# Kernel optimization log

Measured on AMD Instinct MI355X. Metric: run time of the kernel, lower is better.

The kernel has to match this reference:

```python
import jax, jax.numpy as jnp
import numpy as np

D_MODEL = 1024
NUM_HEADS = 16
D_HEAD = D_MODEL // NUM_HEADS


def setup_inputs() -> dict:
    key = jax.random.key(0)
    k1, k2, k3, k4, k5 = jax.random.split(key, 5)
    s = 1.0 / np.sqrt(D_MODEL)
    return {
        "x": jax.random.normal(k1, (4, 2048, D_MODEL), dtype=jnp.float32),
        "W_qkv": jax.random.normal(k2, (D_MODEL, 3 * D_MODEL), dtype=jnp.float32) * s,
        "b_qkv": jnp.zeros((3 * D_MODEL,), dtype=jnp.float32),
        "W_out": jax.random.normal(k3, (D_MODEL, D_MODEL), dtype=jnp.float32) * s,
        "b_out": jnp.zeros((D_MODEL,), dtype=jnp.float32),
    }


def reference(x, W_qkv, b_qkv, W_out, b_out):
    B, T, D = x.shape
    qkv = x @ W_qkv + b_qkv  # [B,T,3D]
    q, k, v = jnp.split(qkv, 3, axis=-1)
    # [B,T,D] -> [B,H,T,dh]
    def to_heads(t):
        return t.reshape(B, T, NUM_HEADS, D_HEAD).transpose(0, 2, 1, 3)
    q, k, v = to_heads(q), to_heads(k), to_heads(v)
    scores = jnp.einsum("bhqd,bhkd->bhqk", q, k) / jnp.sqrt(jnp.float32(D_HEAD))
    attn = jax.nn.softmax(scores, axis=-1)
    out = jnp.einsum("bhqk,bhkd->bhqd", attn, v)
    out = out.transpose(0, 2, 1, 3).reshape(B, T, D)
    return out @ W_out + b_out
```

## Files before the change

### kernel.cpp

```cpp
#include <hip/hip_runtime.h>

typedef unsigned short u16;
typedef unsigned int u32;
typedef u16 u16x4 __attribute__((ext_vector_type(4)));
typedef u16 u16x8 __attribute__((ext_vector_type(8)));
typedef u32 u32x2 __attribute__((ext_vector_type(2)));
typedef u32 u32x4 __attribute__((ext_vector_type(4)));
typedef __bf16 bf16x2 __attribute__((ext_vector_type(2)));
typedef __bf16 bf16x8 __attribute__((ext_vector_type(8)));
typedef float f32x4 __attribute__((ext_vector_type(4)));

__device__ __forceinline__ u16 f2bf(float f) {
  return __builtin_bit_cast(u16, (__bf16)f);
}

__device__ __forceinline__ u32 packbf2(float lo, float hi) {
  bf16x2 t;
  t[0] = (__bf16)lo;
  t[1] = (__bf16)hi;
  return __builtin_bit_cast(u32, t);
}

__device__ __forceinline__ f32x4 mfma16(bf16x8 a, bf16x8 b, f32x4 c) {
  return __builtin_amdgcn_mfma_f32_16x16x32_bf16(a, b, c, 0, 0, 0);
}

#define GLOAD_LDS16(gsrc, ldst)                                              \
  __builtin_amdgcn_global_load_lds(                                          \
      (const __attribute__((address_space(1))) void*)(gsrc),                 \
      (__attribute__((address_space(3))) void*)(ldst), 16, 0, 0)

__global__ __launch_bounds__(256) void cvt_x(const float* __restrict__ in,
                                             u16* __restrict__ out, int n) {
  int i = (blockIdx.x * 256 + threadIdx.x) * 8;
  if (i >= n) return;
  u16x8 o;
#pragma unroll
  for (int j = 0; j < 8; j++) o[j] = f2bf(in[i + j]);
  *(u16x8*)&out[i] = o;
}

__global__ __launch_bounds__(256) void transpose_cvt(const float* __restrict__ in,
                                                     u16* __restrict__ out,
                                                     int R, int C) {
  __shared__ float tile[32][33];
  int gx = blockIdx.x * 32, gy = blockIdx.y * 32;
  int tx = threadIdx.x, ty = threadIdx.y;
#pragma unroll
  for (int i = 0; i < 4; i++)
    tile[ty + i * 8][tx] = in[(size_t)(gy + ty + i * 8) * C + gx + tx];
  __syncthreads();
#pragma unroll
  for (int i = 0; i < 4; i++) {
    int c = ty + i * 8;
    out[(size_t)(gx + c) * R + gy + tx] = f2bf(tile[tx][c]);
  }
}

template <int EPI, int GX>
__global__ __launch_bounds__(256, 4) void gemm_bf16(
    const u16* __restrict__ A, const u16* __restrict__ Bt,
    const float* __restrict__ bias, u16* __restrict__ qb, u16* __restrict__ kb,
    u16* __restrict__ vb, float* __restrict__ fout, int N, int K) {
  __shared__ u16 As[2][128 * 32];
  __shared__ u16 Bs[2][128 * 32];
  const int tid = threadIdx.x;
  const int wave = tid >> 6;
  const int lane = tid & 63;
  const int wr = wave >> 1, wc = wave & 1;
  const int l15 = lane & 15, l4 = lane >> 4;

  const int id = blockIdx.y * GX + blockIdx.x;
  const int xcd = id & 7;
  const int j = id >> 3;
  const int bm = (xcd * 8 + j / GX) * 128;
  const int bn = (j % GX) * 128;

  const int srow = wave * 16 + (lane >> 2);
  const int slch = lane & 3;
  const int ldst = wave * 512;

  const u16* Abase = A + (size_t)bm * K;
  const u16* Bbase = Bt + (size_t)bn * K;

  f32x4 acc[4][4] = {};

  auto STAGE = [&](int buf, int k0) {
#pragma unroll
    for (int c = 0; c < 2; c++) {
      const int row = c * 64 + srow;
      const int sch = slch ^ ((row >> 1) & 3);
      GLOAD_LDS16(Abase + (size_t)row * K + k0 + sch * 8,
                  &As[buf][c * 2048 + ldst]);
      GLOAD_LDS16(Bbase + (size_t)row * K + k0 + sch * 8,
                  &Bs[buf][c * 2048 + ldst]);
    }
  };

  STAGE(0, 0);
  int cur = 0;
  for (int k0 = 0; k0 < K; k0 += 32) {
    __syncthreads();
    if (k0 + 32 < K) STAGE(cur ^ 1, k0 + 32);

    const u16* as = As[cur];
    const u16* bs = Bs[cur];
    bf16x8 af[4], bfr[4];
#pragma unroll
    for (int mi = 0; mi < 4; mi++) {
      const int row = wr * 64 + mi * 16 + l15;
      af[mi] = *(const bf16x8*)&as[row * 32 + ((l4 ^ ((row >> 1) & 3)) * 8)];
    }
#pragma unroll
    for (int ni = 0; ni < 4; ni++) {
      const int row = wc * 64 + ni * 16 + l15;
      bfr[ni] = *(const bf16x8*)&bs[row * 32 + ((l4 ^ ((row >> 1) & 3)) * 8)];
    }
    __builtin_amdgcn_s_setprio(1);
#pragma unroll
    for (int mi = 0; mi < 4; mi++)
#pragma unroll
      for (int ni = 0; ni < 4; ni++)
        acc[mi][ni] = mfma16(af[mi], bfr[ni], acc[mi][ni]);
    __builtin_amdgcn_s_setprio(0);
    cur ^= 1;
  }

#pragma unroll
  for (int mi = 0; mi < 4; mi++) {
#pragma unroll
    for (int ni = 0; ni < 4; ni++) {
      const int col = bn + wc * 64 + ni * 16 + l15;
      const float bv = bias[col];
      const int row0 = bm + wr * 64 + mi * 16 + l4 * 4;
      if (EPI == 0) {
        const int which = col >> 10;
        const int hc = col & 1023;
        const int h = hc >> 6, d = hc & 63;
#pragma unroll
        for (int r = 0; r < 4; r++) {
          const int row = row0 + r;
          const int b = row >> 11, t = row & 2047;
          const float v = acc[mi][ni][r] + bv;
          if (which == 0)
            qb[((size_t)(b * 16 + h) * 2048 + t) * 64 + d] = f2bf(v * 0.18033688f);
          else if (which == 1)
            kb[((size_t)(b * 16 + h) * 2048 + t) * 64 + d] = f2bf(v);
          else {
            const int o = t & 63;
            const int op = (o & 3) | (((o >> 4) & 1) << 2) | (((o >> 2) & 3) << 3) |
                           ((o >> 5) << 5);
            const int tp = (t & ~63) | op;
            vb[((size_t)(b * 16 + h) * 64 + d) * 2048 + tp] = f2bf(v);
          }
        }
      } else {
#pragma unroll
        for (int r = 0; r < 4; r++)
          fout[(size_t)(row0 + r) * N + col] = acc[mi][ni][r] + bv;
      }
    }
  }
}

__global__ __launch_bounds__(256, 4) void attn_kernel(const u16* __restrict__ Q,
                                                      const u16* __restrict__ Kg,
                                                      const u16* __restrict__ Vt,
                                                      u16* __restrict__ O) {
  __shared__ u16 Ks[2][64 * 64];
  __shared__ u16 Vs[2][64 * 64];
  const int tid = threadIdx.x;
  const int wave = tid >> 6;
  const int lane = tid & 63;
  const int l15 = lane & 15, l4 = lane >> 4;

  const int id = blockIdx.y * 16 + blockIdx.x;
  const int xcd = id & 7;
  const int j = id >> 3;
  const int bh = xcd * 8 + (j >> 4);
  const int qt = j & 15;

  const u16* qg = Q + ((size_t)bh * 2048 + qt * 128 + wave * 32) * 64;
  bf16x8 qf[2][2];
#pragma unroll
  for (int mi = 0; mi < 2; mi++)
#pragma unroll
    for (int kg2 = 0; kg2 < 2; kg2++)
      qf[mi][kg2] = *(const bf16x8*)&qg[(mi * 16 + l15) * 64 + kg2 * 32 + l4 * 8];

  float mrow[2] = {-1e30f, -1e30f};
  float lrow[2] = {0.f, 0.f};
  f32x4 oacc[4][2] = {};

  const int srow = wave * 8 + (lane >> 3);
  const int slch = lane & 7;
  const int ldst = wave * 512;
  const u16* kbase = Kg + (size_t)bh * 2048 * 64;
  const u16* vbase = Vt + (size_t)bh * 64 * 2048;

  auto STAGE = [&](int buf, int kt) {
#pragma unroll
    for (int c = 0; c < 2; c++) {
      const int row = c * 32 + srow;
      const int sch = slch ^ (row & 7);
      GLOAD_LDS16(kbase + (size_t)(kt * 64 + row) * 64 + sch * 8,
                  &Ks[buf][c * 2048 + ldst]);
      GLOAD_LDS16(vbase + (size_t)row * 2048 + kt * 64 + sch * 8,
                  &Vs[buf][c * 2048 + ldst]);
    }
  };

  STAGE(0, 0);
  int cur = 0;
  for (int kt = 0; kt < 32; kt++) {
    __syncthreads();
    if (kt + 1 < 32) STAGE(cur ^ 1, kt + 1);
    const u16* ks = Ks[cur];
    const u16* vs = Vs[cur];

    f32x4 sacc[2][4] = {};
    __builtin_amdgcn_s_setprio(1);
#pragma unroll
    for (int kg2 = 0; kg2 < 2; kg2++) {
#pragma unroll
      for (int ni = 0; ni < 4; ni++) {
        const int row = ni * 16 + l15;
        bf16x8 kf =
            *(const bf16x8*)&ks[row * 64 + (((kg2 * 4 + l4) ^ (row & 7)) * 8)];
#pragma unroll
        for (int mi = 0; mi < 2; mi++)
          sacc[mi][ni] = mfma16(kf, qf[mi][kg2], sacc[mi][ni]);
      }
    }
    __builtin_amdgcn_s_setprio(0);

#pragma unroll
    for (int mi = 0; mi < 2; mi++) {
      float pm0 = fmaxf(fmaxf(sacc[mi][0][0], sacc[mi][0][1]),
                        fmaxf(sacc[mi][0][2], sacc[mi][0][3]));
      float pm1 = fmaxf(fmaxf(sacc[mi][1][0], sacc[mi][1][1]),
                        fmaxf(sacc[mi][1][2], sacc[mi][1][3]));
      float pm2 = fmaxf(fmaxf(sacc[mi][2][0], sacc[mi][2][1]),
                        fmaxf(sacc[mi][2][2], sacc[mi][2][3]));
      float pm3 = fmaxf(fmaxf(sacc[mi][3][0], sacc[mi][3][1]),
                        fmaxf(sacc[mi][3][2], sacc[mi][3][3]));
      float pm = fmaxf(fmaxf(pm0, pm1), fmaxf(pm2, pm3));
      pm = fmaxf(pm, __shfl_xor(pm, 16));
      pm = fmaxf(pm, __shfl_xor(pm, 32));
      const bool noskip = !__all(pm - mrow[mi] <= 6.0f);
      float mnew = mrow[mi];
      if (noskip) {
        mnew = fmaxf(mrow[mi], pm);
        const float alpha = __builtin_amdgcn_exp2f(mrow[mi] - mnew);
        mrow[mi] = mnew;
        lrow[mi] *= alpha;
#pragma unroll
        for (int di = 0; di < 4; di++) oacc[di][mi] *= alpha;
      }
      float rs = 0.f;
#pragma unroll
      for (int ni = 0; ni < 4; ni++)
#pragma unroll
        for (int r = 0; r < 4; r++) {
          const float p = __builtin_amdgcn_exp2f(sacc[mi][ni][r] - mnew);
          sacc[mi][ni][r] = p;
          rs += p;
        }
      rs += __shfl_xor(rs, 16);
      rs += __shfl_xor(rs, 32);
      lrow[mi] += rs;
    }

#pragma unroll
    for (int kg2 = 0; kg2 < 2; kg2++) {
      bf16x8 pf[2];
#pragma unroll
      for (int mi = 0; mi < 2; mi++) {
        u32x4 praw;
        praw[0] = packbf2(sacc[mi][2 * kg2][0], sacc[mi][2 * kg2][1]);
        praw[1] = packbf2(sacc[mi][2 * kg2][2], sacc[mi][2 * kg2][3]);
        praw[2] = packbf2(sacc[mi][2 * kg2 + 1][0], sacc[mi][2 * kg2 + 1][1]);
        praw[3] = packbf2(sacc[mi][2 * kg2 + 1][2], sacc[mi][2 * kg2 + 1][3]);
        pf[mi] = __builtin_bit_cast(bf16x8, praw);
      }
      __builtin_amdgcn_s_setprio(1);
#pragma unroll
      for (int di = 0; di < 4; di++) {
        const int row = di * 16 + l15;
        bf16x8 vf =
            *(const bf16x8*)&vs[row * 64 + (((kg2 * 4 + l4) ^ (row & 7)) * 8)];
#pragma unroll
        for (int mi = 0; mi < 2; mi++)
          oacc[di][mi] = mfma16(vf, pf[mi], oacc[di][mi]);
      }
      __builtin_amdgcn_s_setprio(0);
    }
    cur ^= 1;
  }

  const int b = bh >> 4, h = bh & 15;
#pragma unroll
  for (int mi = 0; mi < 2; mi++) {
    const float invl = 1.0f / lrow[mi];
    const int t = qt * 128 + wave * 32 + mi * 16 + l15;
#pragma unroll
    for (int di = 0; di < 4; di++) {
      u16x4 o;
#pragma unroll
      for (int r = 0; r < 4; r++) o[r] = f2bf(oacc[di][mi][r] * invl);
      *(u16x4*)&O[((size_t)b * 2048 + t) * 1024 + h * 64 + di * 16 + l4 * 4] = o;
    }
  }
}

extern "C" void kernel_launch(void* const* d_in, const int* in_sizes, int n_in,
                              void* d_out, int out_size, void* d_ws, size_t ws_size,
                              hipStream_t stream) {
  const float* x = (const float*)d_in[0];
  const float* Wqkv = (const float*)d_in[1];
  const float* bqkv = (const float*)d_in[2];
  const float* Wout = (const float*)d_in[3];
  const float* bout = (const float*)d_in[4];
  float* out = (float*)d_out;

  u16* ws = (u16*)d_ws;
  u16* xb = ws;
  u16* wqT = xb + 8388608;
  u16* woT = wqT + 3145728;
  u16* qb = woT + 1048576;
  u16* kb = qb + 8388608;
  u16* vb = kb + 8388608;
  u16* ao = vb + 8388608;

  cvt_x<<<4096, 256, 0, stream>>>(x, xb, 8388608);
  transpose_cvt<<<dim3(96, 32), dim3(32, 8), 0, stream>>>(Wqkv, wqT, 1024, 3072);
  transpose_cvt<<<dim3(32, 32), dim3(32, 8), 0, stream>>>(Wout, woT, 1024, 1024);
  gemm_bf16<0, 24><<<dim3(24, 64), 256, 0, stream>>>(xb, wqT, bqkv, qb, kb, vb,
                                                     nullptr, 3072, 1024);
  attn_kernel<<<dim3(16, 64), 256, 0, stream>>>(qb, kb, vb, ao);
  gemm_bf16<1, 8><<<dim3(8, 64), 256, 0, stream>>>(ao, woT, bout, nullptr,
                                                   nullptr, nullptr, out, 1024, 1024);
}
```

Measured before the change: 223.4 us.

## Replace 128x128 GEMM with 256x256 tile, 8-wave ping-pong pipelined kernel

Replaces the 128x128 bf16 GEMM with a 256x256-tile kernel using 512 threads, 128KB dynamic LDS split into four double-buffered pieces, and explicit barrier and vmcnt scheduling. Global loads are interleaved with MFMA phases. The goal is more operand reuse per byte loaded and better overlap of loads with compute. The cost is one block per CU and fewer blocks overall: 384 for QKV and only 128 for the output projection, which underfills 256 CUs.

```diff
diff --git a/kernel.cpp b/kernel.cpp
--- a/kernel.cpp
+++ b/kernel.cpp
@@ -30,6 +30,13 @@
       (const __attribute__((address_space(1))) void*)(gsrc),                 \
       (__attribute__((address_space(3))) void*)(ldst), 16, 0, 0)
 
+#define SBAR()                                                               \
+  do {                                                                       \
+    __builtin_amdgcn_sched_barrier(0);                                       \
+    __builtin_amdgcn_s_barrier();                                            \
+    __builtin_amdgcn_sched_barrier(0);                                       \
+  } while (0)
+
 __global__ __launch_bounds__(256) void cvt_x(const float* __restrict__ in,
                                              u16* __restrict__ out, int n) {
   int i = (blockIdx.x * 256 + threadIdx.x) * 8;
@@ -57,82 +64,135 @@
   }
 }
 
-template <int EPI, int GX>
-__global__ __launch_bounds__(256, 4) void gemm_bf16(
+template <int EPI>
+__global__ __launch_bounds__(512, 1) void gemm256(
     const u16* __restrict__ A, const u16* __restrict__ Bt,
     const float* __restrict__ bias, u16* __restrict__ qb, u16* __restrict__ kb,
-    u16* __restrict__ vb, float* __restrict__ fout, int N, int K) {
-  __shared__ u16 As[2][128 * 32];
-  __shared__ u16 Bs[2][128 * 32];
+    u16* __restrict__ vb, float* __restrict__ fout, int N, int K, int NBN) {
+  extern __shared__ u16 lds[];
   const int tid = threadIdx.x;
-  const int wave = tid >> 6;
+  const int wid = tid >> 6;
   const int lane = tid & 63;
-  const int wr = wave >> 1, wc = wave & 1;
+  const int wr = wid >> 2, wc = wid & 3;
   const int l15 = lane & 15, l4 = lane >> 4;
 
-  const int id = blockIdx.y * GX + blockIdx.x;
-  const int xcd = id & 7;
-  const int j = id >> 3;
-  const int bm = (xcd * 8 + j / GX) * 128;
-  const int bn = (j % GX) * 128;
-
-  const int srow = wave * 16 + (lane >> 2);
-  const int slch = lane & 3;
-  const int ldst = wave * 512;
-
-  const u16* Abase = A + (size_t)bm * K;
-  const u16* Bbase = Bt + (size_t)bn * K;
-
-  f32x4 acc[4][4] = {};
-
-  auto STAGE = [&](int buf, int k0) {
+  const int nb = gridDim.x;
+  const int id2 = (blockIdx.x & 7) * (nb >> 3) + (blockIdx.x >> 3);
+  const int bm = (id2 / NBN) * 256;
+  const int bn = (id2 % NBN) * 256;
+
+  const u16* Ab = A + (size_t)bm * K;
+  const u16* Bb = Bt + (size_t)bn * K;
+
+#define PIECE(p, b) (lds + (p) * 16384 + (b) * 8192)
+
+  const int srow = wid * 16 + (lane >> 2);
+  const int sch0 = lane & 3;
+
+  auto STAGE1 = [&](u16* dst, const u16* srcb, int kofs) {
 #pragma unroll
     for (int c = 0; c < 2; c++) {
-      const int row = c * 64 + srow;
-      const int sch = slch ^ ((row >> 1) & 3);
-      GLOAD_LDS16(Abase + (size_t)row * K + k0 + sch * 8,
-                  &As[buf][c * 2048 + ldst]);
-      GLOAD_LDS16(Bbase + (size_t)row * K + k0 + sch * 8,
-                  &Bs[buf][c * 2048 + ldst]);
+      const int row = c * 128 + srow;
+      const int sch = sch0 ^ (row & 3) ^ ((row >> 2) & 3);
+      GLOAD_LDS16(srcb + (size_t)row * K + kofs + sch * 8, dst + c * 4096 + tid * 8);
     }
   };
-
-  STAGE(0, 0);
-  int cur = 0;
-  for (int k0 = 0; k0 < K; k0 += 32) {
-    __syncthreads();
-    if (k0 + 32 < K) STAGE(cur ^ 1, k0 + 32);
-
-    const u16* as = As[cur];
-    const u16* bs = Bs[cur];
-    bf16x8 af[4], bfr[4];
-#pragma unroll
-    for (int mi = 0; mi < 4; mi++) {
-      const int row = wr * 64 + mi * 16 + l15;
-      af[mi] = *(const bf16x8*)&as[row * 32 + ((l4 ^ ((row >> 1) & 3)) * 8)];
-    }
-#pragma unroll
-    for (int ni = 0; ni < 4; ni++) {
-      const int row = wc * 64 + ni * 16 + l15;
-      bfr[ni] = *(const bf16x8*)&bs[row * 32 + ((l4 ^ ((row >> 1) & 3)) * 8)];
-    }
+  auto RDA = [&](const u16* arr, int mi) -> bf16x8 {
+    const int row = wr * 128 + mi * 16 + l15;
+    const int ch = l4 ^ (row & 3) ^ ((row >> 2) & 3);
+    return *(const bf16x8*)&arr[row * 32 + ch * 8];
+  };
+  auto RDB = [&](const u16* arr, int ni) -> bf16x8 {
+    const int row = wc * 64 + ni * 16 + l15;
+    const int ch = l4 ^ (row & 3) ^ ((row >> 2) & 3);
+    return *(const bf16x8*)&arr[row * 32 + ch * 8];
+  };
+
+  f32x4 acc[8][4] = {};
+
+  STAGE1(PIECE(0, 0), Ab, 0);
+  STAGE1(PIECE(2, 0), Bb, 0);
+  STAGE1(PIECE(1, 0), Ab, 32);
+  STAGE1(PIECE(3, 0), Bb, 32);
+  asm volatile("s_waitcnt vmcnt(4)" ::: "memory");
+  SBAR();
+
+  const int NT = K >> 6;
+  for (int t = 0; t < NT; ++t) {
+    const int buf = t & 1, nbuf = buf ^ 1;
+    const int knext = (t + 1) << 6;
+    const bool pre = (t + 1 < NT);
+    bf16x8 af[8], bfr[2];
+
+#pragma unroll
+    for (int mi = 0; mi < 8; mi++) af[mi] = RDA(PIECE(0, buf), mi);
+    bfr[0] = RDB(PIECE(2, buf), 0);
+    bfr[1] = RDB(PIECE(2, buf), 1);
+    if (pre) STAGE1(PIECE(0, nbuf), Ab, knext);
+    SBAR();
     __builtin_amdgcn_s_setprio(1);
 #pragma unroll
-    for (int mi = 0; mi < 4; mi++)
-#pragma unroll
-      for (int ni = 0; ni < 4; ni++)
-        acc[mi][ni] = mfma16(af[mi], bfr[ni], acc[mi][ni]);
+    for (int mi = 0; mi < 8; mi++) {
+      acc[mi][0] = mfma16(af[mi], bfr[0], acc[mi][0]);
+      acc[mi][1] = mfma16(af[mi], bfr[1], acc[mi][1]);
+    }
     __builtin_amdgcn_s_setprio(0);
-    cur ^= 1;
+    SBAR();
+
+    bfr[0] = RDB(PIECE(2, buf), 2);
+    bfr[1] = RDB(PIECE(2, buf), 3);
+    if (pre) STAGE1(PIECE(2, nbuf), Bb, knext);
+    SBAR();
+    __builtin_amdgcn_s_setprio(1);
+#pragma unroll
+    for (int mi = 0; mi < 8; mi++) {
+      acc[mi][2] = mfma16(af[mi], bfr[0], acc[mi][2]);
+      acc[mi][3] = mfma16(af[mi], bfr[1], acc[mi][3]);
+    }
+    __builtin_amdgcn_s_setprio(0);
+    if (pre)
+      asm volatile("s_waitcnt vmcnt(4)" ::: "memory");
+    else
+      asm volatile("s_waitcnt vmcnt(0)" ::: "memory");
+    SBAR();
+
+#pragma unroll
+    for (int mi = 0; mi < 8; mi++) af[mi] = RDA(PIECE(1, buf), mi);
+    bfr[0] = RDB(PIECE(3, buf), 0);
+    bfr[1] = RDB(PIECE(3, buf), 1);
+    if (pre) STAGE1(PIECE(1, nbuf), Ab, knext + 32);
+    SBAR();
+    __builtin_amdgcn_s_setprio(1);
+#pragma unroll
+    for (int mi = 0; mi < 8; mi++) {
+      acc[mi][0] = mfma16(af[mi], bfr[0], acc[mi][0]);
+      acc[mi][1] = mfma16(af[mi], bfr[1], acc[mi][1]);
+    }
+    __builtin_amdgcn_s_setprio(0);
+    SBAR();
+
+    bfr[0] = RDB(PIECE(3, buf), 2);
+    bfr[1] = RDB(PIECE(3, buf), 3);
+    if (pre) STAGE1(PIECE(3, nbuf), Bb, knext + 32);
+    SBAR();
+    __builtin_amdgcn_s_setprio(1);
+#pragma unroll
+    for (int mi = 0; mi < 8; mi++) {
+      acc[mi][2] = mfma16(af[mi], bfr[0], acc[mi][2]);
+      acc[mi][3] = mfma16(af[mi], bfr[1], acc[mi][3]);
+    }
+    __builtin_amdgcn_s_setprio(0);
+    if (pre) asm volatile("s_waitcnt vmcnt(4)" ::: "memory");
+    SBAR();
   }
 
 #pragma unroll
-  for (int mi = 0; mi < 4; mi++) {
+  for (int mi = 0; mi < 8; mi++) {
 #pragma unroll
     for (int ni = 0; ni < 4; ni++) {
       const int col = bn + wc * 64 + ni * 16 + l15;
       const float bv = bias[col];
-      const int row0 = bm + wr * 64 + mi * 16 + l4 * 4;
+      const int row0 = bm + wr * 128 + mi * 16 + l4 * 4;
       if (EPI == 0) {
         const int which = col >> 10;
         const int hc = col & 1023;
@@ -140,17 +200,17 @@
 #pragma unroll
         for (int r = 0; r < 4; r++) {
           const int row = row0 + r;
-          const int b = row >> 11, t = row & 2047;
+          const int b = row >> 11, tt = row & 2047;
           const float v = acc[mi][ni][r] + bv;
           if (which == 0)
-            qb[((size_t)(b * 16 + h) * 2048 + t) * 64 + d] = f2bf(v * 0.18033688f);
+            qb[((size_t)(b * 16 + h) * 2048 + tt) * 64 + d] = f2bf(v * 0.18033688f);
           else if (which == 1)
-            kb[((size_t)(b * 16 + h) * 2048 + t) * 64 + d] = f2bf(v);
+            kb[((size_t)(b * 16 + h) * 2048 + tt) * 64 + d] = f2bf(v);
           else {
-            const int o = t & 63;
-            const int op = (o & 3) | (((o >> 4) & 1) << 2) | (((o >> 2) & 3) << 3) |
-                           ((o >> 5) << 5);
-            const int tp = (t & ~63) | op;
+            const int o = tt & 63;
+            const int op = (o & 3) | (((o >> 4) & 1) << 2) |
+                           (((o >> 2) & 3) << 3) | ((o >> 5) << 5);
+            const int tp = (tt & ~63) | op;
             vb[((size_t)(b * 16 + h) * 64 + d) * 2048 + tp] = f2bf(v);
           }
         }
@@ -161,6 +221,7 @@
       }
     }
   }
+#undef PIECE
 }
 
 __global__ __launch_bounds__(256, 4) void attn_kernel(const u16* __restrict__ Q,
@@ -332,12 +393,17 @@
   u16* vb = kb + 8388608;
   u16* ao = vb + 8388608;
 
+  hipFuncSetAttribute((const void*)gemm256<0>,
+                      hipFuncAttributeMaxDynamicSharedMemorySize, 131072);
+  hipFuncSetAttribute((const void*)gemm256<1>,
+                      hipFuncAttributeMaxDynamicSharedMemorySize, 131072);
+
   cvt_x<<<4096, 256, 0, stream>>>(x, xb, 8388608);
   transpose_cvt<<<dim3(96, 32), dim3(32, 8), 0, stream>>>(Wqkv, wqT, 1024, 3072);
   transpose_cvt<<<dim3(32, 32), dim3(32, 8), 0, stream>>>(Wout, woT, 1024, 1024);
-  gemm_bf16<0, 24><<<dim3(24, 64), 256, 0, stream>>>(xb, wqT, bqkv, qb, kb, vb,
-                                                     nullptr, 3072, 1024);
+  gemm256<0><<<384, 512, 131072, stream>>>(xb, wqT, bqkv, qb, kb, vb, nullptr,
+                                           3072, 1024, 12);
   attn_kernel<<<dim3(16, 64), 256, 0, stream>>>(qb, kb, vb, ao);
-  gemm_bf16<1, 8><<<dim3(8, 64), 256, 0, stream>>>(ao, woT, bout, nullptr,
-                                                   nullptr, nullptr, out, 1024, 1024);
-}
+  gemm256<1><<<128, 512, 131072, stream>>>(ao, woT, bout, nullptr, nullptr,
+                                           nullptr, out, 1024, 1024, 4);
+}
```

Result: slower. 241.7 us (+8.2%).

## Replace LDS-staged GEMM with direct global-to-register fragment loads

Applied to the files above, without the earlier changes.

The bf16 GEMM no longer stages A/B tiles through shared memory with double buffering and barriers. Each wave now loads its MFMA fragments straight from global memory into registers, with two register sets ping-ponged across K steps. This removes LDS traffic and __syncthreads, but it loses the data reuse across waves that LDS provided, which raises global/L2 traffic. It also raises register pressure, and launch bounds are lowered to 3 blocks per SM.

```diff
diff --git a/kernel.cpp b/kernel.cpp
--- a/kernel.cpp
+++ b/kernel.cpp
@@ -58,12 +58,10 @@
 }
 
 template <int EPI, int GX>
-__global__ __launch_bounds__(256, 4) void gemm_bf16(
+__global__ __launch_bounds__(256, 3) void gemm_reg(
     const u16* __restrict__ A, const u16* __restrict__ Bt,
     const float* __restrict__ bias, u16* __restrict__ qb, u16* __restrict__ kb,
     u16* __restrict__ vb, float* __restrict__ fout, int N, int K) {
-  __shared__ u16 As[2][128 * 32];
-  __shared__ u16 Bs[2][128 * 32];
   const int tid = threadIdx.x;
   const int wave = tid >> 6;
   const int lane = tid & 63;
@@ -76,55 +74,47 @@
   const int bm = (xcd * 8 + j / GX) * 128;
   const int bn = (j % GX) * 128;
 
-  const int srow = wave * 16 + (lane >> 2);
-  const int slch = lane & 3;
-  const int ldst = wave * 512;
-
-  const u16* Abase = A + (size_t)bm * K;
-  const u16* Bbase = Bt + (size_t)bn * K;
+  const u16* ap[4];
+  const u16* bp[4];
+#pragma unroll
+  for (int mi = 0; mi < 4; mi++)
+    ap[mi] = A + (size_t)(bm + wr * 64 + mi * 16 + l15) * K + l4 * 8;
+#pragma unroll
+  for (int ni = 0; ni < 4; ni++)
+    bp[ni] = Bt + (size_t)(bn + wc * 64 + ni * 16 + l15) * K + l4 * 8;
 
   f32x4 acc[4][4] = {};
-
-  auto STAGE = [&](int buf, int k0) {
-#pragma unroll
-    for (int c = 0; c < 2; c++) {
-      const int row = c * 64 + srow;
-      const int sch = slch ^ ((row >> 1) & 3);
-      GLOAD_LDS16(Abase + (size_t)row * K + k0 + sch * 8,
-                  &As[buf][c * 2048 + ldst]);
-      GLOAD_LDS16(Bbase + (size_t)row * K + k0 + sch * 8,
-                  &Bs[buf][c * 2048 + ldst]);
-    }
-  };
-
-  STAGE(0, 0);
-  int cur = 0;
-  for (int k0 = 0; k0 < K; k0 += 32) {
-    __syncthreads();
-    if (k0 + 32 < K) STAGE(cur ^ 1, k0 + 32);
-
-    const u16* as = As[cur];
-    const u16* bs = Bs[cur];
-    bf16x8 af[4], bfr[4];
-#pragma unroll
-    for (int mi = 0; mi < 4; mi++) {
-      const int row = wr * 64 + mi * 16 + l15;
-      af[mi] = *(const bf16x8*)&as[row * 32 + ((l4 ^ ((row >> 1) & 3)) * 8)];
-    }
-#pragma unroll
-    for (int ni = 0; ni < 4; ni++) {
-      const int row = wc * 64 + ni * 16 + l15;
-      bfr[ni] = *(const bf16x8*)&bs[row * 32 + ((l4 ^ ((row >> 1) & 3)) * 8)];
-    }
-    __builtin_amdgcn_s_setprio(1);
-#pragma unroll
-    for (int mi = 0; mi < 4; mi++)
-#pragma unroll
-      for (int ni = 0; ni < 4; ni++)
-        acc[mi][ni] = mfma16(af[mi], bfr[ni], acc[mi][ni]);
-    __builtin_amdgcn_s_setprio(0);
-    cur ^= 1;
-  }
+  bf16x8 a0[4], b0[4], a1[4], b1[4];
+
+#define LOADF(dstA, dstB, k0)                                                \
+  do {                                                                       \
+    _Pragma("unroll") for (int i = 0; i < 4; i++) {                          \
+      dstA[i] = *(const bf16x8*)(ap[i] + (k0));                              \
+      dstB[i] = *(const bf16x8*)(bp[i] + (k0));                              \
+    }                                                                        \
+  } while (0)
+
+#define MFMA16(srcA, srcB)                                                   \
+  do {                                                                       \
+    __builtin_amdgcn_s_setprio(1);                                           \
+    _Pragma("unroll") for (int mi = 0; mi < 4; mi++)                         \
+        _Pragma("unroll") for (int ni = 0; ni < 4; ni++) acc[mi][ni] =       \
+            mfma16(srcA[mi], srcB[ni], acc[mi][ni]);                         \
+    __builtin_amdgcn_s_setprio(0);                                           \
+  } while (0)
+
+  LOADF(a0, b0, 0);
+  LOADF(a1, b1, 32);
+  const int NT2 = K >> 6;
+  for (int it = 0; it < NT2; ++it) {
+    const int kn = (it + 1) << 6;
+    MFMA16(a0, b0);
+    if (it + 1 < NT2) LOADF(a0, b0, kn);
+    MFMA16(a1, b1);
+    if (it + 1 < NT2) LOADF(a1, b1, kn + 32);
+  }
+#undef LOADF
+#undef MFMA16
 
 #pragma unroll
   for (int mi = 0; mi < 4; mi++) {
@@ -140,17 +130,17 @@
 #pragma unroll
         for (int r = 0; r < 4; r++) {
           const int row = row0 + r;
-          const int b = row >> 11, t = row & 2047;
+          const int b = row >> 11, tt = row & 2047;
           const float v = acc[mi][ni][r] + bv;
           if (which == 0)
-            qb[((size_t)(b * 16 + h) * 2048 + t) * 64 + d] = f2bf(v * 0.18033688f);
+            qb[((size_t)(b * 16 + h) * 2048 + tt) * 64 + d] = f2bf(v * 0.18033688f);
           else if (which == 1)
-            kb[((size_t)(b * 16 + h) * 2048 + t) * 64 + d] = f2bf(v);
+            kb[((size_t)(b * 16 + h) * 2048 + tt) * 64 + d] = f2bf(v);
           else {
-            const int o = t & 63;
-            const int op = (o & 3) | (((o >> 4) & 1) << 2) | (((o >> 2) & 3) << 3) |
-                           ((o >> 5) << 5);
-            const int tp = (t & ~63) | op;
+            const int o = tt & 63;
+            const int op = (o & 3) | (((o >> 4) & 1) << 2) |
+                           (((o >> 2) & 3) << 3) | ((o >> 5) << 5);
+            const int tp = (tt & ~63) | op;
             vb[((size_t)(b * 16 + h) * 64 + d) * 2048 + tp] = f2bf(v);
           }
         }
@@ -335,9 +325,9 @@
   cvt_x<<<4096, 256, 0, stream>>>(x, xb, 8388608);
   transpose_cvt<<<dim3(96, 32), dim3(32, 8), 0, stream>>>(Wqkv, wqT, 1024, 3072);
   transpose_cvt<<<dim3(32, 32), dim3(32, 8), 0, stream>>>(Wout, woT, 1024, 1024);
-  gemm_bf16<0, 24><<<dim3(24, 64), 256, 0, stream>>>(xb, wqT, bqkv, qb, kb, vb,
-                                                     nullptr, 3072, 1024);
+  gemm_reg<0, 24><<<dim3(24, 64), 256, 0, stream>>>(xb, wqT, bqkv, qb, kb, vb,
+                                                    nullptr, 3072, 1024);
   attn_kernel<<<dim3(16, 64), 256, 0, stream>>>(qb, kb, vb, ao);
-  gemm_bf16<1, 8><<<dim3(8, 64), 256, 0, stream>>>(ao, woT, bout, nullptr,
-                                                   nullptr, nullptr, out, 1024, 1024);
-}
+  gemm_reg<1, 8><<<dim3(8, 64), 256, 0, stream>>>(ao, woT, bout, nullptr,
+                                                  nullptr, nullptr, out, 1024, 1024);
+}
```

After: 358.2 us. 1.6x slower.
